# Optimization experiments

Hardware: AMD Instinct MI355X
Metric: run time of the kernel (lower is better)

## Reference

```python
import jax, jax.numpy as jnp
import numpy as np

N_NODES = 50000
HEADS = 8
NEG_SLOPE = 0.2


def _gat_conv(x, W, a_src, a_dst, b, src, dst, n_nodes):
    """PyG GATConv forward, concat=False (mean over heads), self-loops already in (src, dst)."""
    H, C = a_src.shape
    xl = (x @ W).reshape(n_nodes, H, C)                      # [N, H, C]
    alpha_src = jnp.einsum('nhc,hc->nh', xl, a_src)          # [N, H]
    alpha_dst = jnp.einsum('nhc,hc->nh', xl, a_dst)          # [N, H]
    alpha = jax.nn.leaky_relu(alpha_src[src] + alpha_dst[dst], NEG_SLOPE)  # [E, H]
    # segment softmax over edges grouped by destination node
    amax = jax.ops.segment_max(alpha, dst, num_segments=n_nodes)           # [N, H]
    amax = jnp.where(jnp.isfinite(amax), amax, jnp.zeros_like(amax))
    ex = jnp.exp(alpha - jax.lax.stop_gradient(amax)[dst])                  # [E, H]
    denom = jax.ops.segment_sum(ex, dst, num_segments=n_nodes)             # [N, H]
    coef = ex / (denom[dst] + 1e-16)                                        # [E, H]
    msg = xl[src] * coef[:, :, None]                                        # [E, H, C]
    out = jax.ops.segment_sum(msg, dst, num_segments=n_nodes)              # [N, H, C]
    return out.mean(axis=1) + b                                             # [N, C]


def setup_inputs() -> dict:
    key = jax.random.key(0)
    ks = jax.random.split(key, 12)
    in_feats, h_feats, out_feats = 256, 64, 64
    n_edges = 800000
    x = jax.random.normal(ks[0], (N_NODES, in_feats), dtype=jnp.float32)
    edge_index = jax.random.randint(ks[1], (2, n_edges), 0, N_NODES, dtype=jnp.int64)
    # Glorot-ish init for weights
    def glorot(k, shape, fan):
        return jax.random.normal(k, shape, dtype=jnp.float32) * (1.0 / np.sqrt(fan))
    W1 = glorot(ks[2], (in_feats, HEADS * h_feats), in_feats)
    a_src1 = glorot(ks[3], (HEADS, h_feats), h_feats)
    a_dst1 = glorot(ks[4], (HEADS, h_feats), h_feats)
    b1 = jnp.zeros((h_feats,), dtype=jnp.float32)
    W2 = glorot(ks[5], (h_feats, HEADS * out_feats), h_feats)
    a_src2 = glorot(ks[6], (HEADS, out_feats), out_feats)
    a_dst2 = glorot(ks[7], (HEADS, out_feats), out_feats)
    b2 = jnp.zeros((out_feats,), dtype=jnp.float32)
    return {"x": x, "edge_index": edge_index,
            "W1": W1, "a_src1": a_src1, "a_dst1": a_dst1, "b1": b1,
            "W2": W2, "a_src2": a_src2, "a_dst2": a_dst2, "b2": b2}


def reference(x, edge_index, W1, a_src1, a_dst1, b1, W2, a_src2, a_dst2, b2):
    n = x.shape[0]
    # PyG GATConv add_self_loops=True (default): append self loops
    loops = jnp.arange(n, dtype=edge_index.dtype)
    src = jnp.concatenate([edge_index[0], loops])
    dst = jnp.concatenate([edge_index[1], loops])
    # F.dropout(p=0.6) is identity in eval mode
    h = _gat_conv(x, W1, a_src1, a_dst1, b1, src, dst, n)
    h = jax.nn.relu(h)
    out = _gat_conv(h, W2, a_src2, a_dst2, b2, src, dst, n)
    return out
```

## Files before the change

kernel.cpp:

```cpp
#include <hip/hip_runtime.h>

#define NN 50000
#define HD 8
#define CD 64
#define NHF 512
#define SCAN_B 256
#define NBLK ((NN + SCAN_B - 1) / SCAN_B)

typedef __attribute__((ext_vector_type(8))) short short8v;
typedef __attribute__((ext_vector_type(8))) unsigned short us8;
typedef __attribute__((ext_vector_type(4))) unsigned short us4;
typedef __attribute__((ext_vector_type(4))) float f32x4;
typedef __attribute__((ext_vector_type(4))) _Float16 h4;

__device__ inline unsigned short f32_to_bf16(float f) {
    unsigned int u = __float_as_uint(f);
    unsigned int r = (u + 0x7fffu + ((u >> 16) & 1u)) >> 16;
    return (unsigned short)r;
}
__device__ inline float bf16_to_f32(unsigned short h) {
    return __uint_as_float(((unsigned int)h) << 16);
}

__global__ void k_init_cnt(int* __restrict__ cnt) {
    int i = blockIdx.x * 256 + threadIdx.x;
    if (i < NN) cnt[i] = 1;
}

__global__ void k_hist(const int* __restrict__ dst, int E, int* __restrict__ cnt) {
    int e = blockIdx.x * 256 + threadIdx.x;
    if (e < E) atomicAdd(&cnt[dst[e]], 1);
}

__global__ __launch_bounds__(SCAN_B) void k_block_sums(const int* __restrict__ cnt,
                                                       int* __restrict__ bsums) {
    __shared__ int sdata[4];
    int i = blockIdx.x * SCAN_B + threadIdx.x;
    int v = (i < NN) ? cnt[i] : 0;
#pragma unroll
    for (int off = 1; off < 64; off <<= 1) v += __shfl_xor(v, off);
    if ((threadIdx.x & 63) == 0) sdata[threadIdx.x >> 6] = v;
    __syncthreads();
    if (threadIdx.x == 0) bsums[blockIdx.x] = sdata[0] + sdata[1] + sdata[2] + sdata[3];
}

__global__ __launch_bounds__(SCAN_B) void k_scan_bsums(const int* __restrict__ bsums,
                                                       int* __restrict__ boffs, int nblk) {
    __shared__ int tmp[SCAN_B];
    int tid = threadIdx.x;
    int v = (tid < nblk) ? bsums[tid] : 0;
    tmp[tid] = v;
    __syncthreads();
    for (int off = 1; off < SCAN_B; off <<= 1) {
        int t = (tid >= off) ? tmp[tid - off] : 0;
        __syncthreads();
        tmp[tid] += t;
        __syncthreads();
    }
    if (tid < nblk) boffs[tid] = tmp[tid] - v;
}

__global__ __launch_bounds__(SCAN_B) void k_emit(const int* __restrict__ cnt,
                                                 const int* __restrict__ boffs,
                                                 int* __restrict__ row_ptr,
                                                 int* __restrict__ cursor,
                                                 int* __restrict__ csr_src) {
    __shared__ int tmp[SCAN_B];
    int tid = threadIdx.x;
    int i = blockIdx.x * SCAN_B + tid;
    int v = (i < NN) ? cnt[i] : 0;
    tmp[tid] = v;
    __syncthreads();
    for (int off = 1; off < SCAN_B; off <<= 1) {
        int t = (tid >= off) ? tmp[tid - off] : 0;
        __syncthreads();
        tmp[tid] += t;
        __syncthreads();
    }
    int base = boffs[blockIdx.x] + tmp[tid] - v;
    if (i < NN) {
        row_ptr[i] = base;
        csr_src[base] = i;
        cursor[i] = base + 1;
        if (i == NN - 1) row_ptr[NN] = base + v;
    }
}

__global__ void k_scatter(const int* __restrict__ src, const int* __restrict__ dst,
                          int E, int* __restrict__ cursor, int* __restrict__ csr_src) {
    int e = blockIdx.x * 256 + threadIdx.x;
    if (e < E) {
        int pos = atomicAdd(&cursor[dst[e]], 1);
        csr_src[pos] = src[e];
    }
}

__global__ void k_split_bt(const float* __restrict__ B, unsigned short* __restrict__ bht,
                           unsigned short* __restrict__ blt, int K) {
    int idx = blockIdx.x * 256 + threadIdx.x;
    if (idx < K * NHF) {
        int k = idx >> 9, n = idx & 511;
        float v = B[idx];
        unsigned short hb = f32_to_bf16(v);
        float l = v - bf16_to_f32(hb);
        unsigned short lb = f32_to_bf16(l);
        bht[n * K + k] = hb;
        blt[n * K + k] = lb;
    }
}

#define BM 128
#define BN 128
#define BKF 32
#define LDK 40

__global__ __launch_bounds__(256) void k_gemm_mfma(
    const float* __restrict__ A,
    const unsigned short* __restrict__ Bht,
    const unsigned short* __restrict__ Blt,
    const float* __restrict__ a_src, const float* __restrict__ a_dst,
    _Float16* __restrict__ C, float* __restrict__ asrc_out, float* __restrict__ adst_out,
    int M, int K)
{
    __shared__ unsigned short Ash[BM][LDK];
    __shared__ unsigned short Asl[BM][LDK];
    __shared__ unsigned short Bsh[BN][LDK];
    __shared__ unsigned short Bsl[BN][LDK];

    const int t = threadIdx.x;
    const int lane = t & 63;
    const int wid = t >> 6;
    const int wr = wid >> 1, wc = wid & 1;
    const int bm = blockIdx.x * BM;
    const int bn = blockIdx.y * BN;
    const int l15 = lane & 15;
    const int lg = lane >> 4;

    f32x4 acc[4][4];
#pragma unroll
    for (int mi = 0; mi < 4; ++mi)
#pragma unroll
        for (int ni = 0; ni < 4; ++ni)
            acc[mi][ni] = (f32x4){0.f, 0.f, 0.f, 0.f};

    const int srow = t >> 1;
    const int skc = (t & 1) * 16;

    for (int k0 = 0; k0 < K; k0 += BKF) {
        __syncthreads();
        {
            const int gr = bm + srow;
            if (gr < M) {
                const float* ga = A + (size_t)gr * K + k0 + skc;
#pragma unroll
                for (int c = 0; c < 16; c += 4) {
                    float4 v = *(const float4*)(ga + c);
                    us4 hs, ls;
                    hs.x = f32_to_bf16(v.x); ls.x = f32_to_bf16(v.x - bf16_to_f32(hs.x));
                    hs.y = f32_to_bf16(v.y); ls.y = f32_to_bf16(v.y - bf16_to_f32(hs.y));
                    hs.z = f32_to_bf16(v.z); ls.z = f32_to_bf16(v.z - bf16_to_f32(hs.z));
                    hs.w = f32_to_bf16(v.w); ls.w = f32_to_bf16(v.w - bf16_to_f32(hs.w));
                    *(us4*)&Ash[srow][skc + c] = hs;
                    *(us4*)&Asl[srow][skc + c] = ls;
                }
            } else {
                us4 z = (us4){0, 0, 0, 0};
#pragma unroll
                for (int c = 0; c < 16; c += 4) {
                    *(us4*)&Ash[srow][skc + c] = z;
                    *(us4*)&Asl[srow][skc + c] = z;
                }
            }
            const unsigned short* gbh = Bht + (size_t)(bn + srow) * K + k0 + skc;
            const unsigned short* gbl = Blt + (size_t)(bn + srow) * K + k0 + skc;
            *(us8*)&Bsh[srow][skc] = *(const us8*)gbh;
            *(us8*)&Bsh[srow][skc + 8] = *(const us8*)(gbh + 8);
            *(us8*)&Bsl[srow][skc] = *(const us8*)gbl;
            *(us8*)&Bsl[srow][skc + 8] = *(const us8*)(gbl + 8);
        }
        __syncthreads();

        short8v ah[4], al[4], bh[4], bl[4];
#pragma unroll
        for (int i = 0; i < 4; ++i) {
            ah[i] = *(const short8v*)&Ash[wr * 64 + i * 16 + l15][lg * 8];
            al[i] = *(const short8v*)&Asl[wr * 64 + i * 16 + l15][lg * 8];
            bh[i] = *(const short8v*)&Bsh[wc * 64 + i * 16 + l15][lg * 8];
            bl[i] = *(const short8v*)&Bsl[wc * 64 + i * 16 + l15][lg * 8];
        }
#pragma unroll
        for (int mi = 0; mi < 4; ++mi)
#pragma unroll
            for (int ni = 0; ni < 4; ++ni) {
                acc[mi][ni] = __builtin_amdgcn_mfma_f32_16x16x32_bf16(ah[mi], bh[ni], acc[mi][ni], 0, 0, 0);
                acc[mi][ni] = __builtin_amdgcn_mfma_f32_16x16x32_bf16(ah[mi], bl[ni], acc[mi][ni], 0, 0, 0);
                acc[mi][ni] = __builtin_amdgcn_mfma_f32_16x16x32_bf16(al[mi], bh[ni], acc[mi][ni], 0, 0, 0);
            }
    }

    const int head_w = (bn >> 6) + wc;
    float ca[4], cd[4];
#pragma unroll
    for (int ni = 0; ni < 4; ++ni) {
        ca[ni] = a_src[head_w * 64 + ni * 16 + l15];
        cd[ni] = a_dst[head_w * 64 + ni * 16 + l15];
    }
#pragma unroll
    for (int mi = 0; mi < 4; ++mi) {
#pragma unroll
        for (int r = 0; r < 4; ++r) {
            int row = bm + wr * 64 + mi * 16 + lg * 4 + r;
            float ps = 0.f, pd = 0.f;
#pragma unroll
            for (int ni = 0; ni < 4; ++ni) {
                float cv = acc[mi][ni][r];
                int col = bn + wc * 64 + ni * 16 + l15;
                if (row < M) C[(size_t)row * NHF + col] = (_Float16)cv;
                ps += cv * ca[ni];
                pd += cv * cd[ni];
            }
#pragma unroll
            for (int off = 1; off < 16; off <<= 1) {
                ps += __shfl_xor(ps, off);
                pd += __shfl_xor(pd, off);
            }
            if (l15 == 0 && row < M) {
                asrc_out[row * HD + head_w] = ps;
                adst_out[row * HD + head_w] = pd;
            }
        }
    }
}

__device__ inline void fma4(float4& a, float p, const float4 v) {
    a.x += p * v.x; a.y += p * v.y; a.z += p * v.z; a.w += p * v.w;
}
__device__ inline float4 h4tof4(h4 v) {
    float4 f;
    f.x = (float)v.x; f.y = (float)v.y; f.z = (float)v.z; f.w = (float)v.w;
    return f;
}

__global__ __launch_bounds__(256) void k_aggregate(
    const _Float16* __restrict__ xl, const float* __restrict__ asrc,
    const float* __restrict__ adst, const int* __restrict__ row_ptr,
    const int* __restrict__ csr_src, const float* __restrict__ bias,
    float* __restrict__ out, int relu)
{
    __shared__ float sh[2][NHF];
    const int wid  = threadIdx.x >> 6;
    const int lane = threadIdx.x & 63;
    const int ns   = wid >> 1;
    const int half = wid & 1;
    const int n    = blockIdx.x * 2 + ns;
    const int head = half * 4 + (lane >> 4);
    const int off  = head * CD + (lane & 15) * 4;

    const float ad = adst[n * HD + head];
    const int e0 = row_ptr[n];
    const int e1 = row_ptr[n + 1];

    float4 accA = {0,0,0,0}, accB = {0,0,0,0};
    float sA = 0.f, sB = 0.f;

    int e = e0;
    for (; e + 8 <= e1; e += 8) {
        int idx[8];
#pragma unroll
        for (int k = 0; k < 8; ++k) idx[k] = csr_src[e + k];
        float av[8];
        h4 v[8];
#pragma unroll
        for (int k = 0; k < 8; ++k) {
            av[k] = asrc[idx[k] * HD + head];
            v[k] = *(const h4*)(xl + (size_t)idx[k] * NHF + off);
        }
#pragma unroll
        for (int k = 0; k < 8; ++k) {
            float a = av[k] + ad;
            float p = __expf(a > 0.f ? a : 0.2f * a);
            float4 vf = h4tof4(v[k]);
            if (k & 1) { sB += p; fma4(accB, p, vf); }
            else       { sA += p; fma4(accA, p, vf); }
        }
    }
    for (; e < e1; ++e) {
        const int i0 = csr_src[e];
        float a = asrc[i0 * HD + head] + ad;
        h4 vv = *(const h4*)(xl + (size_t)i0 * NHF + off);
        float p = __expf(a > 0.f ? a : 0.2f * a);
        sA += p;
        fma4(accA, p, h4tof4(vv));
    }

    const float inv = 1.f / (sA + sB + 1e-16f);
    float4 f;
    f.x = (accA.x + accB.x) * inv;
    f.y = (accA.y + accB.y) * inv;
    f.z = (accA.z + accB.z) * inv;
    f.w = (accA.w + accB.w) * inv;
    *(float4*)&sh[ns][off] = f;
    __syncthreads();

    if (wid < 2) {
        const int node = blockIdx.x * 2 + wid;
        float sum = 0.f;
#pragma unroll
        for (int h2 = 0; h2 < HD; ++h2) sum += sh[wid][h2 * CD + lane];
        float res = sum * 0.125f + bias[lane];
        if (relu) res = fmaxf(res, 0.f);
        out[(size_t)node * CD + lane] = res;
    }
}

extern "C" void kernel_launch(void* const* d_in, const int* in_sizes, int n_in,
                              void* d_out, int out_size, void* d_ws, size_t ws_size,
                              hipStream_t stream) {
    const float* x   = (const float*)d_in[0];
    const int*   ei  = (const int*)d_in[1];
    const float* W1  = (const float*)d_in[2];
    const float* as1 = (const float*)d_in[3];
    const float* ad1 = (const float*)d_in[4];
    const float* b1  = (const float*)d_in[5];
    const float* W2  = (const float*)d_in[6];
    const float* as2 = (const float*)d_in[7];
    const float* ad2 = (const float*)d_in[8];
    const float* b2  = (const float*)d_in[9];

    const int E = in_sizes[1] / 2;
    const int* esrc = ei;
    const int* edst = ei + E;

    char* ws = (char*)d_ws;
    _Float16* xlh  = (_Float16*)ws;
    float* asrc    = (float*)(ws + 102400000);
    float* adst    = (float*)(ws + 104000000);
    float* h       = (float*)(ws + 105600000);
    int*   row_ptr = (int*)  (ws + 118400000);
    int*   cursor  = (int*)  (ws + 118600192);
    int*   csr_src = (int*)  (ws + 118800384);
    unsigned short* Bht1 = (unsigned short*)(ws + 122200832);
    unsigned short* Blt1 = (unsigned short*)(ws + 122463232);
    unsigned short* Bht2 = (unsigned short*)(ws + 122725632);
    unsigned short* Blt2 = (unsigned short*)(ws + 122791424);
    int*   bsums   = (int*)  (ws + 122860032);
    int*   boffs   = (int*)  (ws + 122861056);

    k_init_cnt<<<(NN + 255) / 256, 256, 0, stream>>>(cursor);
    k_hist<<<(E + 255) / 256, 256, 0, stream>>>(edst, E, cursor);
    k_block_sums<<<NBLK, SCAN_B, 0, stream>>>(cursor, bsums);
    k_scan_bsums<<<1, SCAN_B, 0, stream>>>(bsums, boffs, NBLK);
    k_emit<<<NBLK, SCAN_B, 0, stream>>>(cursor, boffs, row_ptr, cursor, csr_src);
    k_scatter<<<(E + 255) / 256, 256, 0, stream>>>(esrc, edst, E, cursor, csr_src);

    k_split_bt<<<(256 * NHF + 255) / 256, 256, 0, stream>>>(W1, Bht1, Blt1, 256);
    k_split_bt<<<(64 * NHF + 255) / 256, 256, 0, stream>>>(W2, Bht2, Blt2, 64);

    dim3 gemm_grid((NN + BM - 1) / BM, NHF / BN);

    k_gemm_mfma<<<gemm_grid, 256, 0, stream>>>(x, Bht1, Blt1, as1, ad1, xlh, asrc, adst, NN, 256);
    k_aggregate<<<NN / 2, 256, 0, stream>>>(xlh, asrc, adst, row_ptr, csr_src, b1, h, 1);

    k_gemm_mfma<<<gemm_grid, 256, 0, stream>>>(h, Bht2, Blt2, as2, ad2, xlh, asrc, adst, NN, 64);
    k_aggregate<<<NN / 2, 256, 0, stream>>>(xlh, asrc, adst, row_ptr, csr_src, b2, (float*)d_out, 0);
}
```

Baseline: 470.8 us.

## Pre-split GEMM inputs to bf16 hi/lo and widen aggregation to one wave per node

```diff
diff --git a/kernel.cpp b/kernel.cpp
--- a/kernel.cpp
+++ b/kernel.cpp
@@ -1,6 +1,7 @@
 #include <hip/hip_runtime.h>
 
 #define NN 50000
+#define MPAD 50048
 #define HD 8
 #define CD 64
 #define NHF 512
@@ -11,7 +12,7 @@
 typedef __attribute__((ext_vector_type(8))) unsigned short us8;
 typedef __attribute__((ext_vector_type(4))) unsigned short us4;
 typedef __attribute__((ext_vector_type(4))) float f32x4;
-typedef __attribute__((ext_vector_type(4))) _Float16 h4;
+typedef __attribute__((ext_vector_type(8))) _Float16 h8;
 
 __device__ inline unsigned short f32_to_bf16(float f) {
     unsigned int u = __float_as_uint(f);
@@ -103,10 +104,26 @@
         float v = B[idx];
         unsigned short hb = f32_to_bf16(v);
         float l = v - bf16_to_f32(hb);
-        unsigned short lb = f32_to_bf16(l);
+        blt[n * K + k] = f32_to_bf16(l);
         bht[n * K + k] = hb;
-        blt[n * K + k] = lb;
-    }
+    }
+}
+
+__global__ void k_split_a(const float* __restrict__ A, unsigned short* __restrict__ ah,
+                          unsigned short* __restrict__ al, int M, int K) {
+    int idx = blockIdx.x * 256 + threadIdx.x;
+    int tot = (MPAD * K) >> 2;
+    if (idx >= tot) return;
+    int row = (idx << 2) / K;
+    float4 v = make_float4(0.f, 0.f, 0.f, 0.f);
+    if (row < M) v = *(const float4*)(A + ((size_t)idx << 2));
+    us4 hs, ls;
+    hs.x = f32_to_bf16(v.x); ls.x = f32_to_bf16(v.x - bf16_to_f32(hs.x));
+    hs.y = f32_to_bf16(v.y); ls.y = f32_to_bf16(v.y - bf16_to_f32(hs.y));
+    hs.z = f32_to_bf16(v.z); ls.z = f32_to_bf16(v.z - bf16_to_f32(hs.z));
+    hs.w = f32_to_bf16(v.w); ls.w = f32_to_bf16(v.w - bf16_to_f32(hs.w));
+    *(us4*)(ah + ((size_t)idx << 2)) = hs;
+    *(us4*)(al + ((size_t)idx << 2)) = ls;
 }
 
 #define BM 128
@@ -115,7 +132,8 @@
 #define LDK 40
 
 __global__ __launch_bounds__(256) void k_gemm_mfma(
-    const float* __restrict__ A,
+    const unsigned short* __restrict__ Aht,
+    const unsigned short* __restrict__ Alt,
     const unsigned short* __restrict__ Bht,
     const unsigned short* __restrict__ Blt,
     const float* __restrict__ a_src, const float* __restrict__ a_dst,
@@ -149,33 +167,17 @@
     for (int k0 = 0; k0 < K; k0 += BKF) {
         __syncthreads();
         {
-            const int gr = bm + srow;
-            if (gr < M) {
-                const float* ga = A + (size_t)gr * K + k0 + skc;
-#pragma unroll
-                for (int c = 0; c < 16; c += 4) {
-                    float4 v = *(const float4*)(ga + c);
-                    us4 hs, ls;
-                    hs.x = f32_to_bf16(v.x); ls.x = f32_to_bf16(v.x - bf16_to_f32(hs.x));
-                    hs.y = f32_to_bf16(v.y); ls.y = f32_to_bf16(v.y - bf16_to_f32(hs.y));
-                    hs.z = f32_to_bf16(v.z); ls.z = f32_to_bf16(v.z - bf16_to_f32(hs.z));
-                    hs.w = f32_to_bf16(v.w); ls.w = f32_to_bf16(v.w - bf16_to_f32(hs.w));
-                    *(us4*)&Ash[srow][skc + c] = hs;
-                    *(us4*)&Asl[srow][skc + c] = ls;
-                }
-            } else {
-                us4 z = (us4){0, 0, 0, 0};
-#pragma unroll
-                for (int c = 0; c < 16; c += 4) {
-                    *(us4*)&Ash[srow][skc + c] = z;
-                    *(us4*)&Asl[srow][skc + c] = z;
-                }
-            }
+            const unsigned short* gah = Aht + (size_t)(bm + srow) * K + k0 + skc;
+            const unsigned short* gal = Alt + (size_t)(bm + srow) * K + k0 + skc;
             const unsigned short* gbh = Bht + (size_t)(bn + srow) * K + k0 + skc;
             const unsigned short* gbl = Blt + (size_t)(bn + srow) * K + k0 + skc;
-            *(us8*)&Bsh[srow][skc] = *(const us8*)gbh;
+            *(us8*)&Ash[srow][skc]     = *(const us8*)gah;
+            *(us8*)&Ash[srow][skc + 8] = *(const us8*)(gah + 8);
+            *(us8*)&Asl[srow][skc]     = *(const us8*)gal;
+            *(us8*)&Asl[srow][skc + 8] = *(const us8*)(gal + 8);
+            *(us8*)&Bsh[srow][skc]     = *(const us8*)gbh;
             *(us8*)&Bsh[srow][skc + 8] = *(const us8*)(gbh + 8);
-            *(us8*)&Bsl[srow][skc] = *(const us8*)gbl;
+            *(us8*)&Bsl[srow][skc]     = *(const us8*)gbl;
             *(us8*)&Bsl[srow][skc + 8] = *(const us8*)(gbl + 8);
         }
         __syncthreads();
@@ -232,84 +234,81 @@
     }
 }
 
-__device__ inline void fma4(float4& a, float p, const float4 v) {
-    a.x += p * v.x; a.y += p * v.y; a.z += p * v.z; a.w += p * v.w;
-}
-__device__ inline float4 h4tof4(h4 v) {
-    float4 f;
-    f.x = (float)v.x; f.y = (float)v.y; f.z = (float)v.z; f.w = (float)v.w;
-    return f;
-}
-
 __global__ __launch_bounds__(256) void k_aggregate(
     const _Float16* __restrict__ xl, const float* __restrict__ asrc,
     const float* __restrict__ adst, const int* __restrict__ row_ptr,
     const int* __restrict__ csr_src, const float* __restrict__ bias,
-    float* __restrict__ out, int relu)
+    float* __restrict__ out, unsigned short* __restrict__ o_hi,
+    unsigned short* __restrict__ o_lo, int mode)
 {
-    __shared__ float sh[2][NHF];
+    __shared__ float sh[4][NHF];
     const int wid  = threadIdx.x >> 6;
     const int lane = threadIdx.x & 63;
-    const int ns   = wid >> 1;
-    const int half = wid & 1;
-    const int n    = blockIdx.x * 2 + ns;
-    const int head = half * 4 + (lane >> 4);
-    const int off  = head * CD + (lane & 15) * 4;
+    const int n    = blockIdx.x * 4 + wid;
+    const int head = lane >> 3;
+    const int off  = lane * 8;
 
     const float ad = adst[n * HD + head];
     const int e0 = row_ptr[n];
     const int e1 = row_ptr[n + 1];
 
-    float4 accA = {0,0,0,0}, accB = {0,0,0,0};
-    float sA = 0.f, sB = 0.f;
+    float acc[8] = {};
+    float s = 0.f;
 
     int e = e0;
-    for (; e + 8 <= e1; e += 8) {
-        int idx[8];
-#pragma unroll
-        for (int k = 0; k < 8; ++k) idx[k] = csr_src[e + k];
-        float av[8];
-        h4 v[8];
-#pragma unroll
-        for (int k = 0; k < 8; ++k) {
-            av[k] = asrc[idx[k] * HD + head];
-            v[k] = *(const h4*)(xl + (size_t)idx[k] * NHF + off);
+    for (; e + 4 <= e1; e += 4) {
+        int i0 = csr_src[e];
+        int i1 = csr_src[e + 1];
+        int i2 = csr_src[e + 2];
+        int i3 = csr_src[e + 3];
+        float a0 = asrc[i0 * HD + head];
+        float a1 = asrc[i1 * HD + head];
+        float a2 = asrc[i2 * HD + head];
+        float a3 = asrc[i3 * HD + head];
+        h8 v0 = *(const h8*)(xl + (size_t)i0 * NHF + off);
+        h8 v1 = *(const h8*)(xl + (size_t)i1 * NHF + off);
+        h8 v2 = *(const h8*)(xl + (size_t)i2 * NHF + off);
+        h8 v3 = *(const h8*)(xl + (size_t)i3 * NHF + off);
+        a0 += ad; a1 += ad; a2 += ad; a3 += ad;
+        float p0 = __expf(a0 > 0.f ? a0 : 0.2f * a0);
+        float p1 = __expf(a1 > 0.f ? a1 : 0.2f * a1);
+        float p2 = __expf(a2 > 0.f ? a2 : 0.2f * a2);
+        float p3 = __expf(a3 > 0.f ? a3 : 0.2f * a3);
+        s += p0 + p1 + p2 + p3;
+#pragma unroll
+        for (int j = 0; j < 8; ++j) {
+            acc[j] += p0 * (float)v0[j];
+            acc[j] += p1 * (float)v1[j];
+            acc[j] += p2 * (float)v2[j];
+            acc[j] += p3 * (float)v3[j];
         }
-#pragma unroll
-        for (int k = 0; k < 8; ++k) {
-            float a = av[k] + ad;
-            float p = __expf(a > 0.f ? a : 0.2f * a);
-            float4 vf = h4tof4(v[k]);
-            if (k & 1) { sB += p; fma4(accB, p, vf); }
-            else       { sA += p; fma4(accA, p, vf); }
-        }
     }
     for (; e < e1; ++e) {
-        const int i0 = csr_src[e];
+        int i0 = csr_src[e];
         float a = asrc[i0 * HD + head] + ad;
-        h4 vv = *(const h4*)(xl + (size_t)i0 * NHF + off);
+        h8 vv = *(const h8*)(xl + (size_t)i0 * NHF + off);
         float p = __expf(a > 0.f ? a : 0.2f * a);
-        sA += p;
-        fma4(accA, p, h4tof4(vv));
-    }
-
-    const float inv = 1.f / (sA + sB + 1e-16f);
-    float4 f;
-    f.x = (accA.x + accB.x) * inv;
-    f.y = (accA.y + accB.y) * inv;
-    f.z = (accA.z + accB.z) * inv;
-    f.w = (accA.w + accB.w) * inv;
-    *(float4*)&sh[ns][off] = f;
+        s += p;
+#pragma unroll
+        for (int j = 0; j < 8; ++j) acc[j] += p * (float)vv[j];
+    }
+
+    const float inv = 1.f / (s + 1e-16f);
+#pragma unroll
+    for (int j = 0; j < 8; ++j) sh[wid][off + j] = acc[j] * inv;
     __syncthreads();
 
-    if (wid < 2) {
-        const int node = blockIdx.x * 2 + wid;
-        float sum = 0.f;
-#pragma unroll
-        for (int h2 = 0; h2 < HD; ++h2) sum += sh[wid][h2 * CD + lane];
-        float res = sum * 0.125f + bias[lane];
-        if (relu) res = fmaxf(res, 0.f);
-        out[(size_t)node * CD + lane] = res;
+    float sum = 0.f;
+#pragma unroll
+    for (int h2 = 0; h2 < HD; ++h2) sum += sh[wid][h2 * CD + lane];
+    float res = sum * 0.125f + bias[lane];
+    if (mode) {
+        res = fmaxf(res, 0.f);
+        unsigned short hb = f32_to_bf16(res);
+        o_hi[(size_t)n * CD + lane] = hb;
+        o_lo[(size_t)n * CD + lane] = f32_to_bf16(res - bf16_to_f32(hb));
+    } else {
+        out[(size_t)n * CD + lane] = res;
     }
 }
 
@@ -332,19 +331,22 @@
     const int* edst = ei + E;
 
     char* ws = (char*)d_ws;
-    _Float16* xlh  = (_Float16*)ws;
-    float* asrc    = (float*)(ws + 102400000);
-    float* adst    = (float*)(ws + 104000000);
-    float* h       = (float*)(ws + 105600000);
-    int*   row_ptr = (int*)  (ws + 118400000);
-    int*   cursor  = (int*)  (ws + 118600192);
-    int*   csr_src = (int*)  (ws + 118800384);
-    unsigned short* Bht1 = (unsigned short*)(ws + 122200832);
-    unsigned short* Blt1 = (unsigned short*)(ws + 122463232);
-    unsigned short* Bht2 = (unsigned short*)(ws + 122725632);
-    unsigned short* Blt2 = (unsigned short*)(ws + 122791424);
-    int*   bsums   = (int*)  (ws + 122860032);
-    int*   boffs   = (int*)  (ws + 122861056);
+    _Float16* xlh        = (_Float16*)ws;
+    unsigned short* Ah1  = (unsigned short*)(ws + 51200000);
+    unsigned short* Al1  = (unsigned short*)(ws + 76824576);
+    float* asrc          = (float*)(ws + 102449152);
+    float* adst          = (float*)(ws + 104049152);
+    unsigned short* Hh   = (unsigned short*)(ws + 105649152);
+    unsigned short* Hl   = (unsigned short*)(ws + 112055296);
+    int*   row_ptr       = (int*)(ws + 118461440);
+    int*   cursor        = (int*)(ws + 118661632);
+    int*   csr_src       = (int*)(ws + 118861632);
+    unsigned short* Bht1 = (unsigned short*)(ws + 122261632);
+    unsigned short* Blt1 = (unsigned short*)(ws + 122523776);
+    unsigned short* Bht2 = (unsigned short*)(ws + 122785920);
+    unsigned short* Blt2 = (unsigned short*)(ws + 122851456);
+    int*   bsums         = (int*)(ws + 122916992);
+    int*   boffs         = (int*)(ws + 122917888);
 
     k_init_cnt<<<(NN + 255) / 256, 256, 0, stream>>>(cursor);
     k_hist<<<(E + 255) / 256, 256, 0, stream>>>(edst, E, cursor);
@@ -355,12 +357,17 @@
 
     k_split_bt<<<(256 * NHF + 255) / 256, 256, 0, stream>>>(W1, Bht1, Blt1, 256);
     k_split_bt<<<(64 * NHF + 255) / 256, 256, 0, stream>>>(W2, Bht2, Blt2, 64);
-
-    dim3 gemm_grid((NN + BM - 1) / BM, NHF / BN);
-
-    k_gemm_mfma<<<gemm_grid, 256, 0, stream>>>(x, Bht1, Blt1, as1, ad1, xlh, asrc, adst, NN, 256);
-    k_aggregate<<<NN / 2, 256, 0, stream>>>(xlh, asrc, adst, row_ptr, csr_src, b1, h, 1);
-
-    k_gemm_mfma<<<gemm_grid, 256, 0, stream>>>(h, Bht2, Blt2, as2, ad2, xlh, asrc, adst, NN, 64);
-    k_aggregate<<<NN / 2, 256, 0, stream>>>(xlh, asrc, adst, row_ptr, csr_src, b2, (float*)d_out, 0);
-}
+    k_split_a<<<((MPAD * 256 / 4) + 255) / 256, 256, 0, stream>>>(x, Ah1, Al1, NN, 256);
+
+    dim3 gemm_grid(MPAD / BM, NHF / BN);
+
+    k_gemm_mfma<<<gemm_grid, 256, 0, stream>>>(Ah1, Al1, Bht1, Blt1, as1, ad1,
+                                               xlh, asrc, adst, NN, 256);
+    k_aggregate<<<NN / 4, 256, 0, stream>>>(xlh, asrc, adst, row_ptr, csr_src, b1,
+                                            nullptr, Hh, Hl, 1);
+
+    k_gemm_mfma<<<gemm_grid, 256, 0, stream>>>(Hh, Hl, Bht2, Blt2, as2, ad2,
+                                               xlh, asrc, adst, NN, 64);
+    k_aggregate<<<NN / 4, 256, 0, stream>>>(xlh, asrc, adst, row_ptr, csr_src, b2,
+                                            (float*)d_out, nullptr, nullptr, 0);
+}
```

New measurement: 482.7 us. 2.5% more time.
